# Kernel optimization log

Hardware: AMD Instinct MI355X
Metric: run time of the kernel (lower is better)

Reference implementation:

```python
import jax, jax.numpy as jnp
import numpy as np

N_NODES = 50000


def _gcn_norm(edge_index, n):
    # Add self-loops (PyG GCNConv default) and compute symmetric normalization.
    src = jnp.concatenate([edge_index[0], jnp.arange(n, dtype=edge_index.dtype)])
    dst = jnp.concatenate([edge_index[1], jnp.arange(n, dtype=edge_index.dtype)])
    deg = jax.ops.segment_sum(jnp.ones(src.shape[0], dtype=jnp.float32), dst,
                              num_segments=n)
    dinv = jnp.where(deg > 0, jax.lax.rsqrt(deg), 0.0)
    norm = dinv[src] * dinv[dst]  # [E+N]
    return src, dst, norm


def _gcn_conv(x, src, dst, norm, W, b, n):
    h = x @ W                              # [N, out] linear transform first
    msgs = h[src] * norm[:, None]          # gather + edge-wise scale [E+N, out]
    out = jax.ops.segment_sum(msgs, dst, num_segments=n)  # scatter-add
    return out + b


def setup_inputs() -> dict:
    key = jax.random.key(0)
    k1, k2, k3, k4 = jax.random.split(key, 4)
    N, E, F, H, C = N_NODES, 1600000, 128, 128, 64
    x = jax.random.normal(k1, (N, F), dtype=jnp.float32)
    edge_index = jax.random.randint(k2, (2, E), 0, N, dtype=jnp.int64)
    W1 = jax.random.normal(k3, (F, H), dtype=jnp.float32) * 0.05
    b1 = jnp.zeros((H,), dtype=jnp.float32)
    W2 = jax.random.normal(k4, (H, C), dtype=jnp.float32) * 0.05
    b2 = jnp.zeros((C,), dtype=jnp.float32)
    return {"x": x, "edge_index": edge_index, "W1": W1, "b1": b1,
            "W2": W2, "b2": b2}


def reference(x, edge_index, W1, b1, W2, b2):
    n = x.shape[0]
    src, dst, norm = _gcn_norm(edge_index, n)
    h = _gcn_conv(x, src, dst, norm, W1, b1, n)
    h = jax.nn.relu(h)
    out = _gcn_conv(h, src, dst, norm, W2, b2, n)
    return out
```

## Files before the change

kernel.cpp:

```cpp
#include <hip/hip_runtime.h>
#include <hip/hip_bf16.h>
#include <stdint.h>

#define N_NODES 50000
#define N_EDGES 1600000
#define N_TOT   (N_EDGES + N_NODES)
#define NBKT      256
#define BKT_NODES 196
#define BKT_CAP   7168
#define PBKT_CAP  9216
#define TILE      4096
#define EPT       16
#define ZROW      N_NODES

typedef unsigned short u16;
typedef __attribute__((ext_vector_type(8))) short short8;
typedef __attribute__((ext_vector_type(4))) float floatx4;
typedef __attribute__((ext_vector_type(2))) float f2;

__device__ __forceinline__ float b2f(u16 u) {
    union { unsigned int i; float f; } v; v.i = ((unsigned int)u) << 16; return v.f;
}
__device__ __forceinline__ float asf(unsigned u) {
    union { unsigned int i; float f; } v; v.i = u; return v.f;
}
__device__ __forceinline__ u16 f2b(float f) {
    union { unsigned int i; float f; } v; v.f = f;
    unsigned int r = (v.i + 0x7FFFu + ((v.i >> 16) & 1u)) >> 16;
    return (u16)r;
}

__device__ __forceinline__ void accu(f2& a, unsigned u) {
    f2 r; r.x = asf(u << 16); r.y = asf(u & 0xFFFF0000u);
    a += r;
}
__device__ __forceinline__ void acc4u(f2* a, uint4 q) {
    accu(a[0], q.x); accu(a[1], q.y); accu(a[2], q.z); accu(a[3], q.w);
}
__device__ __forceinline__ void acc2u(f2* a, uint2 q) {
    accu(a[0], q.x); accu(a[1], q.y);
}
__device__ __forceinline__ uint4 g256(const char* hB, unsigned s, unsigned lb) {
    return *(const uint4*)(hB + ((s << 8) + lb));
}
__device__ __forceinline__ uint2 g128(const char* hB, unsigned s, unsigned lb) {
    return *(const uint2*)(hB + ((s << 7) + lb));
}

__global__ __launch_bounds__(256) void k_part(const int* __restrict__ ei,
                                              const unsigned* __restrict__ xw,
                                              int* __restrict__ flags,
                                              unsigned* __restrict__ pairs,
                                              int* __restrict__ bktcnt) {
    __shared__ unsigned pairsL[TILE];
    __shared__ unsigned char bktL[TILE];
    __shared__ int hist[NBKT], incl[NBKT], delta[NBKT];
    __shared__ int zc, pc;
    int tid = threadIdx.x;
    long base = (long)blockIdx.x * TILE;
    hist[tid] = 0;
    if (tid == 0) { zc = 0; pc = 0; }
    __syncthreads();
    unsigned hw = ((const unsigned*)ei)[2 * tid + 1];
    atomicAdd(&zc, hw == 0 ? 1 : 0);
    if (blockIdx.x == 0) {
        unsigned w = xw[tid];
        int ex = (w >> 7) & 0xFF;
        atomicAdd(&pc, ((ex == 0) || (ex >= 0x60 && ex <= 0x9F)) ? 1 : 0);
    }
    __syncthreads();
    int i64 = zc > 250;
    if (blockIdx.x == 0 && tid == 0) {
        flags[0] = (pc < 160) ? 1 : 0;
        flags[1] = i64;
    }

    int myb[EPT], myrank[EPT]; unsigned myp[EPT];
#pragma unroll
    for (int t = 0; t < EPT; t++) {
        long idx = base + t * 256 + tid;
        int b = -1; unsigned p = 0;
        if (idx < N_TOT) {
            int s, d;
            if (idx < N_EDGES) {
                if (i64) { s = ei[2 * idx]; d = ei[2 * (N_EDGES + idx)]; }
                else     { s = ei[idx];     d = ei[N_EDGES + idx]; }
            } else {
                s = d = (int)(idx - N_EDGES);
            }
            b = d / BKT_NODES;
            p = (unsigned)s | ((unsigned)(d - b * BKT_NODES) << 16);
        }
        myb[t] = b; myp[t] = p;
        myrank[t] = (b >= 0) ? atomicAdd(&hist[b], 1) : 0;
    }
    __syncthreads();

    int tot = hist[tid];
    incl[tid] = tot;
    __syncthreads();
    for (int o = 1; o < NBKT; o <<= 1) {
        int t2 = (tid >= o) ? incl[tid - o] : 0;
        __syncthreads();
        incl[tid] += t2;
        __syncthreads();
    }
    int excl = incl[tid] - tot;
    int gb = atomicAdd(&bktcnt[tid], tot);
    hist[tid]  = excl;
    delta[tid] = tid * BKT_CAP + gb - excl;
    __syncthreads();

#pragma unroll
    for (int t = 0; t < EPT; t++) {
        if (myb[t] >= 0) {
            int slot = hist[myb[t]] + myrank[t];
            pairsL[slot] = myp[t];
            bktL[slot]   = (unsigned char)myb[t];
        }
    }
    __syncthreads();
    int count = incl[NBKT - 1];
    for (int i = tid; i < count; i += 256) {
        int b = bktL[i];
        int pos = delta[b] + i;
        if (pos - b * BKT_CAP < BKT_CAP)
            pairs[pos] = pairsL[i];
    }
}

__global__ __launch_bounds__(256) void k_bucket(const unsigned* __restrict__ pairs,
                                                const int* __restrict__ bktcnt,
                                                int* __restrict__ rowstart,
                                                int* __restrict__ deg,
                                                float* __restrict__ dinv,
                                                u16* __restrict__ csr) {
    __shared__ u16 csrL[PBKT_CAP];
    __shared__ int degL[NBKT], curL[NBKT], scanT[NBKT];
    int b = blockIdx.x, tid = threadIdx.x;
    int cnt = bktcnt[b];
    const unsigned* reg = pairs + (size_t)b * BKT_CAP;
    degL[tid] = 0;
    __syncthreads();
    for (int i = tid; i < cnt; i += 256)
        atomicAdd(&degL[reg[i] >> 16], 1);
    __syncthreads();
    int n = b * BKT_NODES + tid;
    int valid = (tid < BKT_NODES) && (n < N_NODES);
    int v = degL[tid];
    int pv = valid ? ((v + 15) & ~15) : 0;
    scanT[tid] = pv;
    __syncthreads();
    for (int o = 1; o < NBKT; o <<= 1) {
        int t = (tid >= o) ? scanT[tid - o] : 0;
        __syncthreads();
        scanT[tid] += t;
        __syncthreads();
    }
    int pexcl = scanT[tid] - pv;
    curL[tid] = pexcl;
    if (valid) {
        rowstart[n] = b * PBKT_CAP + pexcl;
        deg[n]      = v;
        dinv[n]     = rsqrtf((float)v);
    }
    int pcnt = scanT[NBKT - 1];
    if (pcnt > PBKT_CAP) pcnt = PBKT_CAP;
    __syncthreads();
    for (int i = tid; i < pcnt; i += 256) csrL[i] = (u16)ZROW;
    __syncthreads();
    for (int i = tid; i < cnt; i += 256) {
        unsigned p = reg[i];
        int slot = atomicAdd(&curL[p >> 16], 1);
        if (slot < PBKT_CAP) csrL[slot] = (u16)(p & 0xFFFFu);
    }
    __syncthreads();
    for (int i = tid; i < pcnt; i += 256)
        csr[(size_t)b * PBKT_CAP + i] = csrL[i];
}

template<int NOUT, bool ADYN>
__global__ __launch_bounds__(256) void k_gemm(const void* __restrict__ A,
                                              const void* __restrict__ W,
                                              const float* __restrict__ dinv,
                                              u16* __restrict__ out, int M,
                                              const int* __restrict__ flags) {
    const int isf32 = flags[0];
    constexpr int LDW = 136;
    __shared__ __align__(16) u16 Wt[NOUT * LDW];
    int tid = threadIdx.x;
    if (blockIdx.x == 0 && tid < NOUT)
        out[(size_t)M * NOUT + tid] = 0;
    const float* Wf = (const float*)W;
    const u16*   Wu = (const u16*)W;
    for (int idx = tid; idx < 128 * NOUT; idx += 256) {
        int k = idx / NOUT, n = idx % NOUT;
        Wt[n * LDW + k] = isf32 ? f2b(Wf[idx]) : Wu[idx];
    }
    __syncthreads();

    int wave = tid >> 6, lane = tid & 63;
    int quad = lane >> 4, l16 = lane & 15;
    int r0 = blockIdx.x * 64 + wave * 16;
    int r = r0 + l16; if (r >= M) r = M - 1;

    floatx4 acc[NOUT / 16];
#pragma unroll
    for (int i = 0; i < NOUT / 16; i++) acc[i] = (floatx4)(0.f);

#pragma unroll
    for (int ks = 0; ks < 4; ks++) {
        short8 a;
        if (ADYN && isf32) {
            const float* af = (const float*)A + (size_t)r * 128 + ks * 32 + quad * 8;
            float4 v0 = ((const float4*)af)[0];
            float4 v1 = ((const float4*)af)[1];
            a[0] = (short)f2b(v0.x); a[1] = (short)f2b(v0.y);
            a[2] = (short)f2b(v0.z); a[3] = (short)f2b(v0.w);
            a[4] = (short)f2b(v1.x); a[5] = (short)f2b(v1.y);
            a[6] = (short)f2b(v1.z); a[7] = (short)f2b(v1.w);
        } else {
            a = ((const short8*)((const u16*)A + (size_t)r * 128))[ks * 4 + quad];
        }
#pragma unroll
        for (int nt = 0; nt < NOUT / 16; nt++) {
            const short8* bp = (const short8*)&Wt[(nt * 16 + l16) * LDW + ks * 32 + quad * 8];
            acc[nt] = __builtin_amdgcn_mfma_f32_16x16x32_bf16(a, *bp, acc[nt], 0, 0, 0);
        }
    }
    float sc[4];
#pragma unroll
    for (int j = 0; j < 4; j++) {
        int row = r0 + quad * 4 + j;
        sc[j] = dinv[row < M ? row : 0];
    }
#pragma unroll
    for (int nt = 0; nt < NOUT / 16; nt++) {
#pragma unroll
        for (int j = 0; j < 4; j++) {
            int row = r0 + quad * 4 + j;
            if (row < M)
                out[(size_t)row * NOUT + nt * 16 + l16] = f2b(acc[nt][j] * sc[j]);
        }
    }
}

__global__ __launch_bounds__(256) void k_agg1(const u16* __restrict__ h,
                                              const u16* __restrict__ csr,
                                              const int* __restrict__ rowstart,
                                              const int* __restrict__ deg,
                                              const float* __restrict__ dinv,
                                              const void* __restrict__ bias,
                                              u16* __restrict__ out,
                                              const int* __restrict__ flags) {
    int wave = threadIdx.x >> 6, lane = threadIdx.x & 63;
    int d = blockIdx.x * 4 + wave;
    int grp = lane >> 4, l16 = lane & 15;
    int start = rowstart[d], dg = deg[d];
    int pdg = (dg + 15) & ~15;
    int C = pdg >> 2;
    const ushort4* cp = (const ushort4*)(csr + start + grp * C);
    int nc = C >> 2;
    const char* hB = (const char*)h;
    unsigned lb = (unsigned)l16 << 4;

    f2 acc[4] = {};
    ushort4 c = cp[0];
    uint4 q0 = g256(hB, c.x, lb), q1 = g256(hB, c.y, lb),
          q2 = g256(hB, c.z, lb), q3 = g256(hB, c.w, lb);
    for (int k = 1; k < nc; k++) {
        ushort4 cn = cp[k];
        acc4u(acc, q0); q0 = g256(hB, cn.x, lb);
        acc4u(acc, q1); q1 = g256(hB, cn.y, lb);
        acc4u(acc, q2); q2 = g256(hB, cn.z, lb);
        acc4u(acc, q3); q3 = g256(hB, cn.w, lb);
    }
    acc4u(acc, q0); acc4u(acc, q1); acc4u(acc, q2); acc4u(acc, q3);

#pragma unroll
    for (int j = 0; j < 4; j++) {
        acc[j].x += __shfl_xor(acc[j].x, 16); acc[j].y += __shfl_xor(acc[j].y, 16);
        acc[j].x += __shfl_xor(acc[j].x, 32); acc[j].y += __shfl_xor(acc[j].y, 32);
    }
    if (grp == 0) {
        int isf32 = flags[0];
        float dd = dinv[d];
        u16 r8[8];
#pragma unroll
        for (int j = 0; j < 4; j++) {
            float bx = isf32 ? ((const float*)bias)[l16 * 8 + 2 * j]
                             : b2f(((const u16*)bias)[l16 * 8 + 2 * j]);
            float by = isf32 ? ((const float*)bias)[l16 * 8 + 2 * j + 1]
                             : b2f(((const u16*)bias)[l16 * 8 + 2 * j + 1]);
            float vx = acc[j].x * dd + bx;
            float vy = acc[j].y * dd + by;
            r8[2 * j]     = f2b(vx > 0.f ? vx : 0.f);
            r8[2 * j + 1] = f2b(vy > 0.f ? vy : 0.f);
        }
        uint4 o;
        o.x = r8[0] | ((unsigned)r8[1] << 16); o.y = r8[2] | ((unsigned)r8[3] << 16);
        o.z = r8[4] | ((unsigned)r8[5] << 16); o.w = r8[6] | ((unsigned)r8[7] << 16);
        ((uint4*)(out + (size_t)d * 128))[l16] = o;
    }
}

__global__ __launch_bounds__(256) void k_agg2(const u16* __restrict__ h,
                                              const u16* __restrict__ csr,
                                              const int* __restrict__ rowstart,
                                              const int* __restrict__ deg,
                                              const float* __restrict__ dinv,
                                              const void* __restrict__ bias,
                                              float* __restrict__ out,
                                              const int* __restrict__ flags) {
    int wave = threadIdx.x >> 6, lane = threadIdx.x & 63;
    int d = blockIdx.x * 4 + wave;
    int grp = lane >> 4, l16 = lane & 15;
    int start = rowstart[d], dg = deg[d];
    int pdg = (dg + 15) & ~15;
    int C = pdg >> 2;
    const ushort4* cp = (const ushort4*)(csr + start + grp * C);
    int nc = C >> 2;
    const char* hB = (const char*)h;
    unsigned lb = (unsigned)l16 << 3;

    f2 acc[2] = {};
    ushort4 c = cp[0];
    uint2 q0 = g128(hB, c.x, lb), q1 = g128(hB, c.y, lb),
          q2 = g128(hB, c.z, lb), q3 = g128(hB, c.w, lb);
    for (int k = 1; k < nc; k++) {
        ushort4 cn = cp[k];
        acc2u(acc, q0); q0 = g128(hB, cn.x, lb);
        acc2u(acc, q1); q1 = g128(hB, cn.y, lb);
        acc2u(acc, q2); q2 = g128(hB, cn.z, lb);
        acc2u(acc, q3); q3 = g128(hB, cn.w, lb);
    }
    acc2u(acc, q0); acc2u(acc, q1); acc2u(acc, q2); acc2u(acc, q3);

#pragma unroll
    for (int j = 0; j < 2; j++) {
        acc[j].x += __shfl_xor(acc[j].x, 16); acc[j].y += __shfl_xor(acc[j].y, 16);
        acc[j].x += __shfl_xor(acc[j].x, 32); acc[j].y += __shfl_xor(acc[j].y, 32);
    }
    if (grp == 0) {
        int isf32 = flags[0];
        float dd = dinv[d];
        float r4[4];
#pragma unroll
        for (int j = 0; j < 2; j++) {
            float bx = isf32 ? ((const float*)bias)[l16 * 4 + 2 * j]
                             : b2f(((const u16*)bias)[l16 * 4 + 2 * j]);
            float by = isf32 ? ((const float*)bias)[l16 * 4 + 2 * j + 1]
                             : b2f(((const u16*)bias)[l16 * 4 + 2 * j + 1]);
            r4[2 * j]     = acc[j].x * dd + bx;
            r4[2 * j + 1] = acc[j].y * dd + by;
        }
        ((float4*)(out + (size_t)d * 64))[l16] = make_float4(r4[0], r4[1], r4[2], r4[3]);
    }
}

extern "C" void kernel_launch(void* const* d_in, const int* in_sizes, int n_in,
                              void* d_out, int out_size, void* d_ws, size_t ws_size,
                              hipStream_t stream) {
    const void* x  = d_in[0];
    const int*  ei = (const int*)d_in[1];
    const void* W1 = d_in[2];
    const void* b1 = d_in[3];
    const void* W2 = d_in[4];
    const void* b2 = d_in[5];
    float* out = (float*)d_out;

    char* ws = (char*)d_ws;
    int*      flags    = (int*)(ws + 0);
    int*      bktcnt   = (int*)(ws + 1024);
    int*      deg      = (int*)(ws + 4096);
    int*      rowstart = (int*)(ws + 204800);
    float*    dinv     = (float*)(ws + 405504);
    u16*      csr      = (u16*)(ws + 606208);
    unsigned* pairs    = (unsigned*)(ws + 5324800);
    u16*      h1       = (u16*)(ws + 5324800);
    u16*      out1     = (u16*)(ws + 18125056);
    u16*      h2       = (u16*)(ws + 5324800);

    hipMemsetAsync(bktcnt, 0, NBKT * sizeof(int), stream);
    k_part   <<<(N_TOT + TILE - 1) / TILE, 256, 0, stream>>>(ei, (const unsigned*)x,
                                                             flags, pairs, bktcnt);
    k_bucket <<<NBKT, 256, 0, stream>>>(pairs, bktcnt, rowstart, deg, dinv, csr);

    k_gemm<128, true> <<<(N_NODES + 63) / 64, 256, 0, stream>>>(x, W1, dinv, h1, N_NODES, flags);
    k_agg1<<<N_NODES / 4, 256, 0, stream>>>(h1, csr, rowstart, deg, dinv, b1, out1, flags);
    k_gemm<64, false> <<<(N_NODES + 63) / 64, 256, 0, stream>>>(out1, W2, dinv, h2, N_NODES, flags);
    k_agg2<<<N_NODES / 4, 256, 0, stream>>>(h2, csr, rowstart, deg, dinv, b2, out, flags);
}
```

Before: 240.8 us.

## Split feature columns across waves in aggregation kernels to widen edge parallelism

The aggregation kernels now split each destination row's feature vector into 64-byte slices handled by separate blocks: four slices for layer 1 and two for layer 2. Each wave processes sixteen edges at a time with four lanes per edge, instead of four edge groups of sixteen lanes. A block index mapping interleaves the slices so the same nodes' slices run close together in time. This raises the number of gathers in flight per wave and the grid size, at the cost of re-reading the CSR indices once per slice and using shorter, narrower per-lane prefetch pipelines.

Result: slower. 296.1 us (+23.0%).

```diff
diff --git a/kernel.cpp b/kernel.cpp
--- a/kernel.cpp
+++ b/kernel.cpp
@@ -36,15 +36,6 @@
 }
 __device__ __forceinline__ void acc4u(f2* a, uint4 q) {
     accu(a[0], q.x); accu(a[1], q.y); accu(a[2], q.z); accu(a[3], q.w);
-}
-__device__ __forceinline__ void acc2u(f2* a, uint2 q) {
-    accu(a[0], q.x); accu(a[1], q.y);
-}
-__device__ __forceinline__ uint4 g256(const char* hB, unsigned s, unsigned lb) {
-    return *(const uint4*)(hB + ((s << 8) + lb));
-}
-__device__ __forceinline__ uint2 g128(const char* hB, unsigned s, unsigned lb) {
-    return *(const uint2*)(hB + ((s << 7) + lb));
 }
 
 __global__ __launch_bounds__(256) void k_part(const int* __restrict__ ei,
@@ -254,44 +245,47 @@
                                               u16* __restrict__ out,
                                               const int* __restrict__ flags) {
     int wave = threadIdx.x >> 6, lane = threadIdx.x & 63;
-    int d = blockIdx.x * 4 + wave;
-    int grp = lane >> 4, l16 = lane & 15;
+    int k = blockIdx.x & 7;
+    int s = k & 3;
+    int d = (k >> 2) * 25000 + (blockIdx.x >> 3) * 4 + wave;
+    int grp = lane >> 2, lg = lane & 3;
     int start = rowstart[d], dg = deg[d];
-    int pdg = (dg + 15) & ~15;
-    int C = pdg >> 2;
-    const ushort4* cp = (const ushort4*)(csr + start + grp * C);
-    int nc = C >> 2;
+    int R = (dg + 15) >> 4;
+    const u16* cp = csr + start + grp;
     const char* hB = (const char*)h;
-    unsigned lb = (unsigned)l16 << 4;
+    unsigned lb = (unsigned)(s * 64 + lg * 16);
 
     f2 acc[4] = {};
-    ushort4 c = cp[0];
-    uint4 q0 = g256(hB, c.x, lb), q1 = g256(hB, c.y, lb),
-          q2 = g256(hB, c.z, lb), q3 = g256(hB, c.w, lb);
-    for (int k = 1; k < nc; k++) {
-        ushort4 cn = cp[k];
-        acc4u(acc, q0); q0 = g256(hB, cn.x, lb);
-        acc4u(acc, q1); q1 = g256(hB, cn.y, lb);
-        acc4u(acc, q2); q2 = g256(hB, cn.z, lb);
-        acc4u(acc, q3); q3 = g256(hB, cn.w, lb);
-    }
-    acc4u(acc, q0); acc4u(acc, q1); acc4u(acc, q2); acc4u(acc, q3);
+    unsigned ia = cp[0];
+    unsigned ib = cp[(unsigned)((1 < R ? 1 : R - 1) * 16)];
+    uint4 q = *(const uint4*)(hB + ((ia << 8) + lb));
+    for (int r = 1; r < R; r++) {
+        int rn = (r + 1 < R) ? (r + 1) : (R - 1);
+        unsigned ic = cp[(unsigned)(rn * 16)];
+        uint4 qn = *(const uint4*)(hB + ((ib << 8) + lb));
+        acc4u(acc, q);
+        q = qn; ib = ic;
+    }
+    acc4u(acc, q);
 
 #pragma unroll
     for (int j = 0; j < 4; j++) {
+        acc[j].x += __shfl_xor(acc[j].x, 4);  acc[j].y += __shfl_xor(acc[j].y, 4);
+        acc[j].x += __shfl_xor(acc[j].x, 8);  acc[j].y += __shfl_xor(acc[j].y, 8);
         acc[j].x += __shfl_xor(acc[j].x, 16); acc[j].y += __shfl_xor(acc[j].y, 16);
         acc[j].x += __shfl_xor(acc[j].x, 32); acc[j].y += __shfl_xor(acc[j].y, 32);
     }
     if (grp == 0) {
         int isf32 = flags[0];
         float dd = dinv[d];
+        int fb = s * 32 + lg * 8;
         u16 r8[8];
 #pragma unroll
         for (int j = 0; j < 4; j++) {
-            float bx = isf32 ? ((const float*)bias)[l16 * 8 + 2 * j]
-                             : b2f(((const u16*)bias)[l16 * 8 + 2 * j]);
-            float by = isf32 ? ((const float*)bias)[l16 * 8 + 2 * j + 1]
-                             : b2f(((const u16*)bias)[l16 * 8 + 2 * j + 1]);
+            float bx = isf32 ? ((const float*)bias)[fb + 2 * j]
+                             : b2f(((const u16*)bias)[fb + 2 * j]);
+            float by = isf32 ? ((const float*)bias)[fb + 2 * j + 1]
+                             : b2f(((const u16*)bias)[fb + 2 * j + 1]);
             float vx = acc[j].x * dd + bx;
             float vy = acc[j].y * dd + by;
             r8[2 * j]     = f2b(vx > 0.f ? vx : 0.f);
@@ -300,7 +294,7 @@
         uint4 o;
         o.x = r8[0] | ((unsigned)r8[1] << 16); o.y = r8[2] | ((unsigned)r8[3] << 16);
         o.z = r8[4] | ((unsigned)r8[5] << 16); o.w = r8[6] | ((unsigned)r8[7] << 16);
-        ((uint4*)(out + (size_t)d * 128))[l16] = o;
+        *(uint4*)(out + (size_t)d * 128 + fb) = o;
     }
 }
 
@@ -313,48 +307,53 @@
                                               float* __restrict__ out,
                                               const int* __restrict__ flags) {
     int wave = threadIdx.x >> 6, lane = threadIdx.x & 63;
-    int d = blockIdx.x * 4 + wave;
-    int grp = lane >> 4, l16 = lane & 15;
+    int k = blockIdx.x & 7;
+    int s = k & 1;
+    int d = (k >> 1) * 12500 + (blockIdx.x >> 3) * 4 + wave;
+    int grp = lane >> 2, lg = lane & 3;
     int start = rowstart[d], dg = deg[d];
-    int pdg = (dg + 15) & ~15;
-    int C = pdg >> 2;
-    const ushort4* cp = (const ushort4*)(csr + start + grp * C);
-    int nc = C >> 2;
+    int R = (dg + 15) >> 4;
+    const u16* cp = csr + start + grp;
     const char* hB = (const char*)h;
-    unsigned lb = (unsigned)l16 << 3;
-
-    f2 acc[2] = {};
-    ushort4 c = cp[0];
-    uint2 q0 = g128(hB, c.x, lb), q1 = g128(hB, c.y, lb),
-          q2 = g128(hB, c.z, lb), q3 = g128(hB, c.w, lb);
-    for (int k = 1; k < nc; k++) {
-        ushort4 cn = cp[k];
-        acc2u(acc, q0); q0 = g128(hB, cn.x, lb);
-        acc2u(acc, q1); q1 = g128(hB, cn.y, lb);
-        acc2u(acc, q2); q2 = g128(hB, cn.z, lb);
-        acc2u(acc, q3); q3 = g128(hB, cn.w, lb);
-    }
-    acc2u(acc, q0); acc2u(acc, q1); acc2u(acc, q2); acc2u(acc, q3);
-
-#pragma unroll
-    for (int j = 0; j < 2; j++) {
+    unsigned lb = (unsigned)(s * 64 + lg * 16);
+
+    f2 acc[4] = {};
+    unsigned ia = cp[0];
+    unsigned ib = cp[(unsigned)((1 < R ? 1 : R - 1) * 16)];
+    uint4 q = *(const uint4*)(hB + ((ia << 7) + lb));
+    for (int r = 1; r < R; r++) {
+        int rn = (r + 1 < R) ? (r + 1) : (R - 1);
+        unsigned ic = cp[(unsigned)(rn * 16)];
+        uint4 qn = *(const uint4*)(hB + ((ib << 7) + lb));
+        acc4u(acc, q);
+        q = qn; ib = ic;
+    }
+    acc4u(acc, q);
+
+#pragma unroll
+    for (int j = 0; j < 4; j++) {
+        acc[j].x += __shfl_xor(acc[j].x, 4);  acc[j].y += __shfl_xor(acc[j].y, 4);
+        acc[j].x += __shfl_xor(acc[j].x, 8);  acc[j].y += __shfl_xor(acc[j].y, 8);
         acc[j].x += __shfl_xor(acc[j].x, 16); acc[j].y += __shfl_xor(acc[j].y, 16);
         acc[j].x += __shfl_xor(acc[j].x, 32); acc[j].y += __shfl_xor(acc[j].y, 32);
     }
     if (grp == 0) {
         int isf32 = flags[0];
         float dd = dinv[d];
-        float r4[4];
-#pragma unroll
-        for (int j = 0; j < 2; j++) {
-            float bx = isf32 ? ((const float*)bias)[l16 * 4 + 2 * j]
-                             : b2f(((const u16*)bias)[l16 * 4 + 2 * j]);
-            float by = isf32 ? ((const float*)bias)[l16 * 4 + 2 * j + 1]
-                             : b2f(((const u16*)bias)[l16 * 4 + 2 * j + 1]);
-            r4[2 * j]     = acc[j].x * dd + bx;
-            r4[2 * j + 1] = acc[j].y * dd + by;
-        }
-        ((float4*)(out + (size_t)d * 64))[l16] = make_float4(r4[0], r4[1], r4[2], r4[3]);
+        int fb = s * 32 + lg * 8;
+        float r8[8];
+#pragma unroll
+        for (int j = 0; j < 4; j++) {
+            float bx = isf32 ? ((const float*)bias)[fb + 2 * j]
+                             : b2f(((const u16*)bias)[fb + 2 * j]);
+            float by = isf32 ? ((const float*)bias)[fb + 2 * j + 1]
+                             : b2f(((const u16*)bias)[fb + 2 * j + 1]);
+            r8[2 * j]     = acc[j].x * dd + bx;
+            r8[2 * j + 1] = acc[j].y * dd + by;
+        }
+        float4* op = (float4*)(out + (size_t)d * 64 + fb);
+        op[0] = make_float4(r8[0], r8[1], r8[2], r8[3]);
+        op[1] = make_float4(r8[4], r8[5], r8[6], r8[7]);
     }
 }
 
@@ -387,7 +386,7 @@
     k_bucket <<<NBKT, 256, 0, stream>>>(pairs, bktcnt, rowstart, deg, dinv, csr);
 
     k_gemm<128, true> <<<(N_NODES + 63) / 64, 256, 0, stream>>>(x, W1, dinv, h1, N_NODES, flags);
-    k_agg1<<<N_NODES / 4, 256, 0, stream>>>(h1, csr, rowstart, deg, dinv, b1, out1, flags);
+    k_agg1<<<50000, 256, 0, stream>>>(h1, csr, rowstart, deg, dinv, b1, out1, flags);
     k_gemm<64, false> <<<(N_NODES + 63) / 64, 256, 0, stream>>>(out1, W2, dinv, h2, N_NODES, flags);
-    k_agg2<<<N_NODES / 4, 256, 0, stream>>>(h2, csr, rowstart, deg, dinv, b2, out, flags);
-}
+    k_agg2<<<25000, 256, 0, stream>>>(h2, csr, rowstart, deg, dinv, b2, out, flags);
+}
```
